# Kernel optimization log

Measured on AMD Instinct MI355X. Metric: run time of the kernel, lower is better.

The kernel has to match this reference:

```python
import jax, jax.numpy as jnp
import numpy as np

B, M, N = 64, 100, 100
LAMBDA_COORD = 1.0
LAMBDA_CONF = 1.0
EPS = 1e-12


def _hungarian(cost):
    """O(n^3) Hungarian algorithm (potentials / e-maxx variant) on a square
    numpy cost matrix. Returns row_to_col assignment (length n)."""
    n = cost.shape[0]
    u = np.zeros(n + 1)
    v = np.zeros(n + 1)
    p = np.zeros(n + 1, dtype=np.int64)   # p[j] = row matched to column j
    way = np.zeros(n + 1, dtype=np.int64)
    for i in range(1, n + 1):
        p[0] = i
        j0 = 0
        minv = np.full(n + 1, np.inf)
        used = np.zeros(n + 1, dtype=bool)
        while True:
            used[j0] = True
            i0 = p[j0]
            js = np.nonzero(~used)[0]
            js = js[js > 0]
            cur = cost[i0 - 1, js - 1] - u[i0] - v[js]
            upd = cur < minv[js]
            minv[js] = np.where(upd, cur, minv[js])
            way[js] = np.where(upd, j0, way[js])
            j1 = js[np.argmin(minv[js])]
            delta = minv[j1]
            uj = np.nonzero(used)[0]
            u[p[uj]] += delta
            v[uj] -= delta
            minv[js] -= delta
            j0 = j1
            if p[j0] == 0:
                break
        while j0:
            j1 = way[j0]
            p[j0] = p[j1]
            j0 = j1
    row_to_col = np.full(n, -1, dtype=np.int64)
    for j in range(1, n + 1):
        row_to_col[p[j] - 1] = j - 1
    return row_to_col


def _match(pred_xy, target_xy, target_conf):
    """Host-side matching (mirrors the original's CPU round trip).
    Returns padded rows [B,P], cols [B,P] (cols index into the ORIGINAL target
    axis) and cnt [B] = number of matched pairs (min(M, K_valid))."""
    Bb, Mm, _ = pred_xy.shape
    Nn = target_xy.shape[1]
    P = min(Mm, Nn)
    rows = np.zeros((Bb, P), np.int64)
    cols = np.zeros((Bb, P), np.int64)
    cnt = np.zeros(Bb, np.int64)
    for b in range(Bb):
        valid = np.nonzero(target_conf[b] > 0.5)[0]
        K = valid.size
        if K == 0:
            continue
        tgt = target_xy[b, valid]                       # [K,2]
        cost = np.linalg.norm(pred_xy[b][:, None, :] - tgt[None, :, :], axis=-1)  # [M,K]
        n = max(Mm, K)
        sq = np.zeros((n, n))                           # zero-pad to square
        sq[:Mm, :K] = cost
        r2c = _hungarian(sq)
        k = 0
        for r in range(Mm):
            c = r2c[r]
            if 0 <= c < K:
                rows[b, k] = r
                cols[b, k] = valid[c]
                k += 1
        cnt[b] = k
    return rows, cols, cnt


def _loss(pred, target, rows, cols, cnt):
    Bb, P = rows.shape
    bidx = jnp.arange(Bb)[:, None]
    mp = pred[bidx, rows]                                # [B,P,3] matched preds
    mt = target[bidx, cols]                              # [B,P,3] matched tgts
    mask = (jnp.arange(P)[None, :] < cnt[:, None]).astype(pred.dtype)
    denom = jnp.maximum(cnt, 1).astype(pred.dtype)
    # per-batch F.mse_loss: mean over cnt*2 coord elements
    se = (((mp[..., :2] - mt[..., :2]) ** 2).sum(-1) * mask).sum(-1)
    loss_coord = jnp.where(cnt > 0, se / (2.0 * denom), 0.0).sum()
    # per-batch F.binary_cross_entropy: mean over cnt elements
    pconf = jnp.clip(mp[..., 2], EPS, 1.0 - EPS)
    tconf = mt[..., 2]
    bce = -(tconf * jnp.log(pconf) + (1.0 - tconf) * jnp.log1p(-pconf))
    loss_conf = jnp.where(cnt > 0, (bce * mask).sum(-1) / denom, 0.0).sum()
    return (LAMBDA_COORD * loss_coord + LAMBDA_CONF * loss_conf) / Bb


def setup_inputs() -> dict:
    key = jax.random.key(0)
    k1, k2 = jax.random.split(key)
    pred = jax.random.uniform(k1, (B, M, 3), dtype=jnp.float32)
    target = jax.random.uniform(k2, (B, N, 3), dtype=jnp.float32)
    return {"pred": pred, "target": target}


def reference(pred, target):
    pred_np = np.asarray(pred)
    tgt_np = np.asarray(target)
    rows, cols, cnt = _match(pred_np[..., :2], tgt_np[..., :2], tgt_np[..., 2])
    rows = jnp.asarray(rows)
    cols = jnp.asarray(cols)
    cnt = jnp.asarray(cnt)
    return _loss(pred, target, rows, cols, cnt)
```

## Files before the change

### kernel.cpp

```cpp
#include <hip/hip_runtime.h>
#include <math.h>

#define BATCH 64
#define MM 100
#define NN 100
#define ST 101
#define BIGCLAIM 0x7fffffff


__device__ __forceinline__ int readlane_i(int v, int lane) {
    return __builtin_amdgcn_readlane(v, lane);
}
__device__ __forceinline__ float readlane_f(float v, int lane) {
    return __int_as_float(__builtin_amdgcn_readlane(__float_as_int(v), lane));
}
__device__ __forceinline__ double readlane_d(double x, int lane) {
    union { double d; int i[2]; } u; u.d = x;
    union { int i[2]; double d; } r;
    r.i[0] = __builtin_amdgcn_readlane(u.i[0], lane);
    r.i[1] = __builtin_amdgcn_readlane(u.i[1], lane);
    return r.d;
}

template<int CTRL>
__device__ __forceinline__ double dpp_min_f64(double x) {
    union { double d; int i[2]; } u, p;
    u.d = x;
    p.i[0] = __builtin_amdgcn_update_dpp(u.i[0], u.i[0], CTRL, 0xF, 0xF, false);
    p.i[1] = __builtin_amdgcn_update_dpp(u.i[1], u.i[1], CTRL, 0xF, 0xF, false);
    return fmin(u.d, p.d);
}
__device__ __forceinline__ double wave_min_f64(double x) {
    x = dpp_min_f64<0xB1>(x);
    x = dpp_min_f64<0x4E>(x);
    x = dpp_min_f64<0x141>(x);
    x = dpp_min_f64<0x140>(x);
    x = dpp_min_f64<0x142>(x);
    x = dpp_min_f64<0x143>(x);
    return readlane_d(x, 63);
}

template<int CTRL>
__device__ __forceinline__ float dpp_min_f32(float x) {
    int p = __builtin_amdgcn_update_dpp(__float_as_int(x), __float_as_int(x),
                                        CTRL, 0xF, 0xF, false);
    return fminf(x, __int_as_float(p));
}
__device__ __forceinline__ float wave_min_f32(float x) {
    x = dpp_min_f32<0xB1>(x);
    x = dpp_min_f32<0x4E>(x);
    x = dpp_min_f32<0x141>(x);
    x = dpp_min_f32<0x140>(x);
    x = dpp_min_f32<0x142>(x);
    x = dpp_min_f32<0x143>(x);
    return readlane_f(x, 63);
}


__global__ __launch_bounds__(128) void hungarian_loss_kernel(
        const float* __restrict__ pred, const float* __restrict__ target,
        double* __restrict__ ws) {
    const int b    = blockIdx.x;
    const int tid  = threadIdx.x;
    const int lane = tid & 63;
    const int wave = tid >> 6;
    const float* P = pred + b * MM * 3;
    const float* T = target + b * NN * 3;

    __shared__ float px[MM], py[MM], pc[MM];
    __shared__ float tvx[NN], tvy[NN], tvc[NN];
    __shared__ float Tc[NN * ST];
    __shared__ float rminv[NN];
    __shared__ int   rmini[NN];
    __shared__ int   claimArr[MM + 1];
    __shared__ int   Ksh;

    float pxA = P[3*lane], pyA = P[3*lane+1];
    float pxB = 0.f, pyB = 0.f;
    const bool colBvalid = (lane + 64 < MM);
    if (colBvalid) { pxB = P[3*(lane+64)]; pyB = P[3*(lane+64)+1]; }

    if (wave == 0) {
        px[lane] = pxA; py[lane] = pyA; pc[lane] = P[3*lane+2];
        if (colBvalid) { px[lane+64]=pxB; py[lane+64]=pyB; pc[lane+64]=P[3*(lane+64)+2]; }
        float cxA=0.f, cyA=0.f, ccA=0.f, cxB=0.f, cyB=0.f, ccB=0.f;
        bool vA_=false, vB_=false;
        { cxA=T[3*lane]; cyA=T[3*lane+1]; ccA=T[3*lane+2]; vA_ = ccA > 0.5f; }
        if (lane + 64 < NN) {
            cxB=T[3*(lane+64)]; cyB=T[3*(lane+64)+1]; ccB=T[3*(lane+64)+2];
            vB_ = ccB > 0.5f;
        }
        unsigned long long mAv = __ballot(vA_);
        unsigned long long mBv = __ballot(vB_);
        int nA_ = __popcll(mAv);
        int K0  = nA_ + __popcll(mBv);
        unsigned long long below = (1ull << lane) - 1ull;
        if (vA_) { int q = __popcll(mAv & below);       tvx[q]=cxA; tvy[q]=cyA; tvc[q]=ccA; }
        if (vB_) { int q = nA_ + __popcll(mBv & below); tvx[q]=cxB; tvy[q]=cyB; tvc[q]=ccB; }
        if (lane == 0) Ksh = K0;
        claimArr[lane] = BIGCLAIM;
        if (lane + 64 <= MM) claimArr[lane + 64] = BIGCLAIM;
    }
    __syncthreads();
    const int K = Ksh;
    if (K == 0) { if (tid == 0) ws[b] = 0.0; return; }

    float txA = (lane < K)      ? tvx[lane]      : 0.f;
    float tyA = (lane < K)      ? tvy[lane]      : 0.f;
    float txB = (lane + 64 < K) ? tvx[lane + 64] : 0.f;
    float tyB = (lane + 64 < K) ? tvy[lane + 64] : 0.f;

    for (int c = wave; c < K; c += 2) {
        float tx = (c < 64) ? readlane_f(txA, c) : readlane_f(txB, c - 64);
        float ty = (c < 64) ? readlane_f(tyA, c) : readlane_f(tyB, c - 64);
        float dxA = __fsub_rn(pxA, tx), dyA = __fsub_rn(pyA, ty);
        float cA = __fsqrt_rn(__fadd_rn(__fmul_rn(dxA,dxA), __fmul_rn(dyA,dyA)));
        Tc[c*ST + lane] = cA;
        float cB = 1e30f;
        if (colBvalid) {
            float dxB = __fsub_rn(pxB, tx), dyB = __fsub_rn(pyB, ty);
            cB = __fsqrt_rn(__fadd_rn(__fmul_rn(dxB,dxB), __fmul_rn(dyB,dyB)));
            Tc[c*ST + lane + 64] = cB;
        }
        float m = wave_min_f32(fminf(cA, cB));
        unsigned long long eA = __ballot(cA == m);
        unsigned long long eB = __ballot(cB == m);
        int argc = eA ? ((int)__ffsll(eA) - 1) : ((int)__ffsll(eB) - 1 + 64);
        if (lane == 0) { rminv[c] = m; rmini[c] = argc; }
    }
    __syncthreads();
    if (wave == 1) return;

    const int jA = lane;
    const int jB = lane + 64;
    const bool validB = (jB <= MM);
    const int idxA = (jA >= 1) ? (jA - 1) : 0;
    const int idxB = validB ? (jB - 1) : (MM - 1);

    int rA = lane + 1, rB = lane + 65;
    int argA = 0, argB = 0;
    if (lane < K)      { argA = rmini[lane] + 1;      atomicMin(&claimArr[argA], rA); }
    if (lane + 64 < K) { argB = rmini[lane + 64] + 1; atomicMin(&claimArr[argB], rB); }
    __threadfence_block();
    int pA = 0, pB = 0;
    if (jA >= 1) { int c0 = claimArr[jA]; pA = (c0 != BIGCLAIM) ? c0 : 0; }
    if (validB)  { int c0 = claimArr[jB]; pB = (c0 != BIGCLAIM) ? c0 : 0; }
    bool freeA = (lane < K)      && (claimArr[argA] != rA);
    bool freeB = (lane + 64 < K) && (claimArr[argB] != rB);
    unsigned long long fA = __ballot(freeA);
    unsigned long long fB = __ballot(freeB);

    double vvA = 0.0, vvB = 0.0;

    const double INF = __builtin_inf();
    while (fA | fB) {
        int r;
        if (fA) { r = (int)__ffsll(fA);      fA &= fA - 1; }
        else    { r = (int)__ffsll(fB) + 64; fB &= fB - 1; }

        double minvA = INF, minvB = INF;
        int wayA = 0, wayB = 0;
        bool usedA = (lane == 0), usedB = false;
        double dpopA = 0.0, dpopB = 0.0;
        if (lane == 0) pA = r;
        int j0 = 0, jfree = -1;
        double dstar = 0.0;

        float cA_f = Tc[(r-1)*ST + idxA];
        float cB_f = Tc[(r-1)*ST + idxB];
        double S = -(double)rminv[r-1];

        for (int it = 0; it <= MM; ++it) {
            double candA = INF, candB = INF;
            if (jA >= 1 && !usedA) {
                double t = ((double)cA_f - vvA) + S;
                if (t < minvA) { minvA = t; wayA = j0; }
                candA = minvA;
            }
            if (validB && !usedB) {
                double t = ((double)cB_f - vvB) + S;
                if (t < minvB) { minvB = t; wayB = j0; }
                candB = minvB;
            }

            double delta = wave_min_f64(fmin(candA, candB));
            unsigned long long eA = __ballot(candA == delta);
            unsigned long long eB = __ballot(candB == delta);
            int j1 = eA ? ((int)__ffsll(eA) - 1) : ((int)__ffsll(eB) - 1 + 64);

            if (jA == j1) { usedA = true; dpopA = delta; }
            if (jB == j1) { usedB = true; dpopB = delta; }

            int pa = readlane_i(pA, j1 & 63);
            int pb = readlane_i(pB, j1 & 63);
            int pj1 = (j1 < 64) ? pa : pb;
            if (pj1 == 0) { jfree = j1; dstar = delta; break; }

            float nxA = Tc[(pj1-1)*ST + idxA];
            float nxB = Tc[(pj1-1)*ST + idxB];
            float cjm = (j1 < 64) ? readlane_f(nxA, j1) : readlane_f(nxB, j1 & 63);
            double vjm = (j1 < 64) ? readlane_d(vvA, j1) : readlane_d(vvB, j1 & 63);
            S = (delta - (double)cjm) + vjm;
            cA_f = nxA; cB_f = nxB;
            j0 = j1;
        }

        if (usedA && jA >= 1) vvA += dpopA - dstar;
        if (usedB)            vvB += dpopB - dstar;

        int jc = jfree;
        for (int s = 0; s <= MM && jc > 0; ++s) {
            int wa = readlane_i(wayA, jc & 63);
            int wb = readlane_i(wayB, jc & 63);
            int w  = (jc < 64) ? wa : wb;
            int pa = readlane_i(pA, w & 63);
            int pb = readlane_i(pB, w & 63);
            int pw = (w < 64) ? pa : pb;
            if (jA == jc) pA = pw;
            if (jB == jc) pB = pw;
            jc = w;
        }
    }

    double se = 0.0, bce = 0.0;
    if (jA >= 1 && pA > 0) {
        int rr = jA - 1, c = pA - 1;
        float dx = __fsub_rn(px[rr], tvx[c]);
        float dy = __fsub_rn(py[rr], tvy[c]);
        se = (double)dx*(double)dx + (double)dy*(double)dy;
        double pcv = (double)pc[rr];
        pcv = fmin(fmax(pcv, 1e-12), 1.0 - 1e-12);
        double tc = (double)tvc[c];
        bce = -(tc * log(pcv) + (1.0 - tc) * log1p(-pcv));
    }
    if (validB && pB > 0) {
        int rr = jB - 1, c = pB - 1;
        float dx = __fsub_rn(px[rr], tvx[c]);
        float dy = __fsub_rn(py[rr], tvy[c]);
        se += (double)dx*(double)dx + (double)dy*(double)dy;
        double pcv = (double)pc[rr];
        pcv = fmin(fmax(pcv, 1e-12), 1.0 - 1e-12);
        double tc = (double)tvc[c];
        bce += -(tc * log(pcv) + (1.0 - tc) * log1p(-pcv));
    }
    for (int m = 1; m < 64; m <<= 1) {
        se  += __shfl_xor(se,  m, 64);
        bce += __shfl_xor(bce, m, 64);
    }
    if (lane == 0) ws[b] = se / (2.0 * (double)K) + bce / (double)K;
}

__global__ __launch_bounds__(64) void final_reduce(const double* __restrict__ ws,
                                                   float* __restrict__ out) {
    double v = ws[threadIdx.x];
    for (int m = 1; m < 64; m <<= 1) v += __shfl_xor(v, m, 64);
    if (threadIdx.x == 0) out[0] = (float)(v / (double)BATCH);
}

extern "C" void kernel_launch(void* const* d_in, const int* in_sizes, int n_in,
                              void* d_out, int out_size, void* d_ws, size_t ws_size,
                              hipStream_t stream) {
    const float* pred   = (const float*)d_in[0];
    const float* target = (const float*)d_in[1];
    double* ws = (double*)d_ws;
    float* out = (float*)d_out;
    hungarian_loss_kernel<<<dim3(BATCH), dim3(128), 0, stream>>>(pred, target, ws);
    final_reduce<<<dim3(1), dim3(64), 0, stream>>>(ws, out);
}
```

Measured before the change: 58.35 us.

## Add auction-style augmenting-row-reduction sweeps before Dijkstra and switch potentials to fp32

Inserts two augmenting row-reduction sweeps, in the style of the Jonker-Volgenant heuristic. Each free row takes its best and second-best reduced columns, lowers that column's potential, and bumps the previous holder back to the free list. Only rows that are still unassigned afterwards go through the full shortest-augmenting-path search, which should cut the number of long serial Dijkstra iterations. All potentials and wave reductions also move from double to float, roughly halving DPP/readlane traffic per step. The cost is extra work per sweep, and fp32 potentials may choose a different assignment than the fp64 reference when costs are near-tied.

```diff
diff --git a/kernel.cpp b/kernel.cpp
--- a/kernel.cpp
+++ b/kernel.cpp
@@ -13,31 +13,6 @@
 }
 __device__ __forceinline__ float readlane_f(float v, int lane) {
     return __int_as_float(__builtin_amdgcn_readlane(__float_as_int(v), lane));
-}
-__device__ __forceinline__ double readlane_d(double x, int lane) {
-    union { double d; int i[2]; } u; u.d = x;
-    union { int i[2]; double d; } r;
-    r.i[0] = __builtin_amdgcn_readlane(u.i[0], lane);
-    r.i[1] = __builtin_amdgcn_readlane(u.i[1], lane);
-    return r.d;
-}
-
-template<int CTRL>
-__device__ __forceinline__ double dpp_min_f64(double x) {
-    union { double d; int i[2]; } u, p;
-    u.d = x;
-    p.i[0] = __builtin_amdgcn_update_dpp(u.i[0], u.i[0], CTRL, 0xF, 0xF, false);
-    p.i[1] = __builtin_amdgcn_update_dpp(u.i[1], u.i[1], CTRL, 0xF, 0xF, false);
-    return fmin(u.d, p.d);
-}
-__device__ __forceinline__ double wave_min_f64(double x) {
-    x = dpp_min_f64<0xB1>(x);
-    x = dpp_min_f64<0x4E>(x);
-    x = dpp_min_f64<0x141>(x);
-    x = dpp_min_f64<0x140>(x);
-    x = dpp_min_f64<0x142>(x);
-    x = dpp_min_f64<0x143>(x);
-    return readlane_d(x, 63);
 }
 
 template<int CTRL>
@@ -70,7 +45,6 @@
     __shared__ float px[MM], py[MM], pc[MM];
     __shared__ float tvx[NN], tvy[NN], tvc[NN];
     __shared__ float Tc[NN * ST];
-    __shared__ float rminv[NN];
     __shared__ int   rmini[NN];
     __shared__ int   claimArr[MM + 1];
     __shared__ int   Ksh;
@@ -126,11 +100,12 @@
         unsigned long long eA = __ballot(cA == m);
         unsigned long long eB = __ballot(cB == m);
         int argc = eA ? ((int)__ffsll(eA) - 1) : ((int)__ffsll(eB) - 1 + 64);
-        if (lane == 0) { rminv[c] = m; rmini[c] = argc; }
+        if (lane == 0) rmini[c] = argc;
     }
     __syncthreads();
     if (wave == 1) return;
 
+    const float INF32 = __builtin_inff();
     const int jA = lane;
     const int jB = lane + 64;
     const bool validB = (jB <= MM);
@@ -150,40 +125,104 @@
     unsigned long long fA = __ballot(freeA);
     unsigned long long fB = __ballot(freeB);
 
-    double vvA = 0.0, vvB = 0.0;
-
-    const double INF = __builtin_inf();
-    while (fA | fB) {
+    float vvA = 0.f, vvB = 0.f;
+
+    unsigned long long dijA = 0ull, dijB = 0ull;
+    for (int sweep = 0; sweep < 2; ++sweep) {
+        unsigned long long curA = fA, curB = fB;
+        fA = 0ull; fB = 0ull;
+        while (curA | curB) {
+            int r;
+            if (curA) { r = (int)__ffsll(curA);      curA &= curA - 1; }
+            else      { r = (int)__ffsll(curB) + 64; curB &= curB - 1; }
+
+            float cA = Tc[(r-1)*ST + idxA];
+            float cB = Tc[(r-1)*ST + idxB];
+            float rcA = (jA >= 1) ? (cA - vvA) : INF32;
+            float rcB = validB ? (cB - vvB) : INF32;
+            float m1 = wave_min_f32(fminf(rcA, rcB));
+            unsigned long long eA = __ballot(rcA == m1);
+            unsigned long long eB = __ballot(rcB == m1);
+            int j1 = eA ? ((int)__ffsll(eA) - 1) : ((int)__ffsll(eB) - 1 + 64);
+
+            float rcA2 = (jA == j1) ? INF32 : rcA;
+            float rcB2 = (jB == j1) ? INF32 : rcB;
+            float m2 = wave_min_f32(fminf(rcA2, rcB2));
+
+            int holder = (j1 < 64) ? readlane_i(pA, j1) : readlane_i(pB, j1 & 63);
+
+            if (m1 < m2) {
+                float dv = m2 - m1;
+                if (jA == j1) { vvA -= dv; pA = r; }
+                if (validB && jB == j1) { vvB -= dv; pB = r; }
+                if (holder != 0) {
+                    if (sweep == 0) {
+                        if (holder <= 64) fA |= 1ull << (holder - 1);
+                        else              fB |= 1ull << (holder - 65);
+                    } else {
+                        if (holder <= 64) dijA |= 1ull << (holder - 1);
+                        else              dijB |= 1ull << (holder - 65);
+                    }
+                }
+            } else {
+                if (holder == 0) {
+                    if (jA == j1) pA = r;
+                    if (validB && jB == j1) pB = r;
+                } else {
+                    unsigned long long e2A = __ballot(rcA2 == m2);
+                    unsigned long long e2B = __ballot(rcB2 == m2);
+                    int j2 = e2A ? ((int)__ffsll(e2A) - 1)
+                                 : ((int)__ffsll(e2B) - 1 + 64);
+                    int h2 = (j2 < 64) ? readlane_i(pA, j2)
+                                       : readlane_i(pB, j2 & 63);
+                    if (h2 == 0) {
+                        if (jA == j2) pA = r;
+                        if (validB && jB == j2) pB = r;
+                    } else {
+                        if (sweep == 0) {
+                            if (r <= 64) fA |= 1ull << (r - 1);
+                            else         fB |= 1ull << (r - 65);
+                        } else {
+                            if (r <= 64) dijA |= 1ull << (r - 1);
+                            else         dijB |= 1ull << (r - 65);
+                        }
+                    }
+                }
+            }
+        }
+    }
+
+    while (dijA | dijB) {
         int r;
-        if (fA) { r = (int)__ffsll(fA);      fA &= fA - 1; }
-        else    { r = (int)__ffsll(fB) + 64; fB &= fB - 1; }
-
-        double minvA = INF, minvB = INF;
+        if (dijA) { r = (int)__ffsll(dijA);      dijA &= dijA - 1; }
+        else      { r = (int)__ffsll(dijB) + 64; dijB &= dijB - 1; }
+
+        float minvA = INF32, minvB = INF32;
         int wayA = 0, wayB = 0;
         bool usedA = (lane == 0), usedB = false;
-        double dpopA = 0.0, dpopB = 0.0;
+        float dpopA = 0.f, dpopB = 0.f;
         if (lane == 0) pA = r;
         int j0 = 0, jfree = -1;
-        double dstar = 0.0;
+        float dstar = 0.f;
 
         float cA_f = Tc[(r-1)*ST + idxA];
         float cB_f = Tc[(r-1)*ST + idxB];
-        double S = -(double)rminv[r-1];
+        float S = 0.f;
 
         for (int it = 0; it <= MM; ++it) {
-            double candA = INF, candB = INF;
+            float candA = INF32, candB = INF32;
             if (jA >= 1 && !usedA) {
-                double t = ((double)cA_f - vvA) + S;
+                float t = (cA_f - vvA) + S;
                 if (t < minvA) { minvA = t; wayA = j0; }
                 candA = minvA;
             }
             if (validB && !usedB) {
-                double t = ((double)cB_f - vvB) + S;
+                float t = (cB_f - vvB) + S;
                 if (t < minvB) { minvB = t; wayB = j0; }
                 candB = minvB;
             }
 
-            double delta = wave_min_f64(fmin(candA, candB));
+            float delta = wave_min_f32(fminf(candA, candB));
             unsigned long long eA = __ballot(candA == delta);
             unsigned long long eB = __ballot(candB == delta);
             int j1 = eA ? ((int)__ffsll(eA) - 1) : ((int)__ffsll(eB) - 1 + 64);
@@ -199,8 +238,8 @@
             float nxA = Tc[(pj1-1)*ST + idxA];
             float nxB = Tc[(pj1-1)*ST + idxB];
             float cjm = (j1 < 64) ? readlane_f(nxA, j1) : readlane_f(nxB, j1 & 63);
-            double vjm = (j1 < 64) ? readlane_d(vvA, j1) : readlane_d(vvB, j1 & 63);
-            S = (delta - (double)cjm) + vjm;
+            float vjm = (j1 < 64) ? readlane_f(vvA, j1) : readlane_f(vvB, j1 & 63);
+            S = (delta - cjm) + vjm;
             cA_f = nxA; cB_f = nxB;
             j0 = j1;
         }
```

Result: faster. 53.63 us (-8.1%).
